# Kernel optimization log

Measured on AMD Instinct MI355X. Metric: run time of the kernel, lower is better.

## Reference

```python
import jax, jax.numpy as jnp
import numpy as np


def setup_inputs() -> dict:
    key = jax.random.key(0)
    k1, k2, k3 = jax.random.split(key, 3)
    n_nodes, d = 1_000_000, 128
    B, L, w, neg_size = 1024, 80, 5, 4
    A = L - w + 1  # 76 anchors per walk
    walk = jax.random.randint(k1, (B, L), 0, n_nodes)
    # torch.randint(low=1, high=n_nodes-1) -> values in [1, n_nodes-2]
    neg = jax.random.randint(k2, (B, A, neg_size), 1, n_nodes - 1)
    embed = jax.random.normal(k3, (n_nodes, d), dtype=jnp.float32)
    return {"walk": walk, "neg": neg, "embed": embed}


def reference(walk, neg, embed):
    B, L = walk.shape
    A = neg.shape[1]          # L - window_size + 1
    w = L - A + 1             # window_size
    anc = walk[:, :A]                                       # [B, A]
    # pos[b, t, i] = walk[b, t + 1 + i], i in [0, w-2]
    sl = jnp.arange(A)[:, None] + jnp.arange(1, w)[None, :]  # [A, w-1]
    pos = walk[:, sl]                                        # [B, A, w-1]
    e_anc = embed[anc]                                       # [B, A, D]
    # fused gather + per-window dot products
    pos_logit = jnp.einsum('bacd,bad->bac', embed[pos], e_anc)  # [B, A, w-1]
    neg_logit = jnp.einsum('bacd,bad->bac', embed[neg], e_anc)  # [B, A, neg]
    # BCEWithLogitsLoss with labels 1 (pos) and 0 (neg), mean over all elements:
    #   label=1 -> softplus(-x);  label=0 -> softplus(x)
    total = pos_logit.size + neg_logit.size
    loss = (jnp.sum(jax.nn.softplus(-pos_logit)) +
            jnp.sum(jax.nn.softplus(neg_logit))) / total
    return loss
```

## Files before the change

### kernel.cpp

```cpp
#include <hip/hip_runtime.h>
#include <math.h>

#define BD   1024
#define LW   80
#define AA   76
#define NEGS 4
#define D    128
#define PAIRS (BD * AA)
#define PAIRS_PER_WAVE 8
#define WAVES_PER_BLOCK 4
#define NBLOCKS (PAIRS / (PAIRS_PER_WAVE * WAVES_PER_BLOCK))

__device__ __forceinline__ float softplus(float x) {
    return fmaxf(x, 0.0f) + log1pf(__expf(-fabsf(x)));
}

__global__ __launch_bounds__(256) void sg_partial(
    const int* __restrict__ walk, const int* __restrict__ neg,
    const float* __restrict__ embed, float* __restrict__ ws)
{
    __shared__ float s_wsum[WAVES_PER_BLOCK];
    const int tid  = threadIdx.x;
    const int wave = tid >> 6;
    const int lane = tid & 63;
    const int gwave = blockIdx.x * WAVES_PER_BLOCK + wave;
    const int pbase = gwave * PAIRS_PER_WAVE;

    float wsum = 0.0f;

    #pragma unroll 1
    for (int i = 0; i < PAIRS_PER_WAVE; ++i) {
        const int p = pbase + i;
        const int b = p / AA;
        const int a = p - b * AA;

        const int* wrow = walk + b * LW + a;
        const int anc = wrow[0];
        const int t0 = wrow[1];
        const int t1 = wrow[2];
        const int t2 = wrow[3];
        const int t3 = wrow[4];
        const int4 nv = *(const int4*)(neg + (size_t)(b * AA + a) * NEGS);

        const size_t loff = (size_t)(lane * 2);
        const float2 ea = *(const float2*)(embed + (size_t)anc * D + loff);

        const float2 e0 = *(const float2*)(embed + (size_t)t0   * D + loff);
        const float2 e1 = *(const float2*)(embed + (size_t)t1   * D + loff);
        const float2 e2 = *(const float2*)(embed + (size_t)t2   * D + loff);
        const float2 e3 = *(const float2*)(embed + (size_t)t3   * D + loff);
        const float2 e4 = *(const float2*)(embed + (size_t)nv.x * D + loff);
        const float2 e5 = *(const float2*)(embed + (size_t)nv.y * D + loff);
        const float2 e6 = *(const float2*)(embed + (size_t)nv.z * D + loff);
        const float2 e7 = *(const float2*)(embed + (size_t)nv.w * D + loff);

        float a0 = fmaf(ea.x, e0.x, ea.y * e0.y);
        float a1 = fmaf(ea.x, e1.x, ea.y * e1.y);
        float a2 = fmaf(ea.x, e2.x, ea.y * e2.y);
        float a3 = fmaf(ea.x, e3.x, ea.y * e3.y);
        float a4 = fmaf(ea.x, e4.x, ea.y * e4.y);
        float a5 = fmaf(ea.x, e5.x, ea.y * e5.y);
        float a6 = fmaf(ea.x, e6.x, ea.y * e6.y);
        float a7 = fmaf(ea.x, e7.x, ea.y * e7.y);

        #pragma unroll
        for (int m = 1; m < 64; m <<= 1) {
            a0 += __shfl_xor(a0, m, 64);
            a1 += __shfl_xor(a1, m, 64);
            a2 += __shfl_xor(a2, m, 64);
            a3 += __shfl_xor(a3, m, 64);
            a4 += __shfl_xor(a4, m, 64);
            a5 += __shfl_xor(a5, m, 64);
            a6 += __shfl_xor(a6, m, 64);
            a7 += __shfl_xor(a7, m, 64);
        }

        wsum += softplus(-a0) + softplus(-a1) + softplus(-a2) + softplus(-a3)
              + softplus( a4) + softplus( a5) + softplus( a6) + softplus( a7);
    }

    if (lane == 0) s_wsum[wave] = wsum;
    __syncthreads();
    if (tid == 0)
        ws[blockIdx.x] = s_wsum[0] + s_wsum[1] + s_wsum[2] + s_wsum[3];
}

__global__ __launch_bounds__(256) void sg_reduce(
    const float* __restrict__ ws, float* __restrict__ out)
{
    __shared__ float s[WAVES_PER_BLOCK];
    const int tid = threadIdx.x;
    float sum = 0.0f;
    for (int i = tid; i < NBLOCKS; i += 256) sum += ws[i];
    #pragma unroll
    for (int m = 1; m < 64; m <<= 1) sum += __shfl_xor(sum, m, 64);
    const int wave = tid >> 6;
    const int lane = tid & 63;
    if (lane == 0) s[wave] = sum;
    __syncthreads();
    if (tid == 0) {
        const float total = (float)((size_t)PAIRS * 8);
        out[0] = (s[0] + s[1] + s[2] + s[3]) * (1.0f / total);
    }
}

extern "C" void kernel_launch(void* const* d_in, const int* in_sizes, int n_in,
                              void* d_out, int out_size, void* d_ws, size_t ws_size,
                              hipStream_t stream) {
    const int*   walk  = (const int*)d_in[0];
    const int*   neg   = (const int*)d_in[1];
    const float* embed = (const float*)d_in[2];
    float* ws  = (float*)d_ws;
    float* out = (float*)d_out;

    sg_partial<<<NBLOCKS, 256, 0, stream>>>(walk, neg, embed, ws);
    sg_reduce<<<1, 256, 0, stream>>>(ws, out);
}
```

Baseline: 651.8 us.

## Map one walk per block and reuse sliding-window embeddings across anchors

Each block now processes a single walk, with each wave handling 19 consecutive anchors and keeping the five window embeddings in a register ring so only one new positive row is gathered per step. The per-pair dot-product reduction is restructured as a transposing butterfly so lanes end up owning one logit each, cutting shuffle count and softplus work per lane. This removes redundant global gathers of overlapping window rows and reduces cross-lane traffic, at the cost of a fully unrolled loop with higher register pressure and less parallel granularity per block.

Measured after the change: 587.7 us. 1.11x faster.

```diff
diff --git a/kernel.cpp b/kernel.cpp
--- a/kernel.cpp
+++ b/kernel.cpp
@@ -7,79 +7,83 @@
 #define NEGS 4
 #define D    128
 #define PAIRS (BD * AA)
-#define PAIRS_PER_WAVE 8
 #define WAVES_PER_BLOCK 4
-#define NBLOCKS (PAIRS / (PAIRS_PER_WAVE * WAVES_PER_BLOCK))
+#define PAIRS_PER_WAVE 19
+#define NBLOCKS BD
 
 __device__ __forceinline__ float softplus(float x) {
     return fmaxf(x, 0.0f) + log1pf(__expf(-fabsf(x)));
 }
 
-__global__ __launch_bounds__(256) void sg_partial(
+__global__ __launch_bounds__(256, 4) void sg_partial(
     const int* __restrict__ walk, const int* __restrict__ neg,
     const float* __restrict__ embed, float* __restrict__ ws)
 {
     __shared__ float s_wsum[WAVES_PER_BLOCK];
     const int tid  = threadIdx.x;
-    const int wave = tid >> 6;
     const int lane = tid & 63;
-    const int gwave = blockIdx.x * WAVES_PER_BLOCK + wave;
-    const int pbase = gwave * PAIRS_PER_WAVE;
+    const int wave = __builtin_amdgcn_readfirstlane(tid >> 6);
+    const int b    = blockIdx.x;
+    const int a0   = wave * PAIRS_PER_WAVE;
+
+    const float* erow = embed + (size_t)(lane * 2);
+    const int*   wrow = walk + b * LW + a0;
+    const int*   nrow = neg + (size_t)(b * AA + a0) * NEGS;
+
+    float2 r[5];
+    #pragma unroll
+    for (int j = 0; j < 5; ++j)
+        r[j] = *(const float2*)(erow + (size_t)wrow[j] * D);
+
+    const bool hi1 = lane & 1;
+    const bool hi2 = lane & 2;
+    const bool hi3 = lane & 4;
 
     float wsum = 0.0f;
 
-    #pragma unroll 1
+    #pragma unroll
     for (int i = 0; i < PAIRS_PER_WAVE; ++i) {
-        const int p = pbase + i;
-        const int b = p / AA;
-        const int a = p - b * AA;
+        const int4 nv = *(const int4*)(nrow + i * NEGS);
+        const float2 e4 = *(const float2*)(erow + (size_t)nv.x * D);
+        const float2 e5 = *(const float2*)(erow + (size_t)nv.y * D);
+        const float2 e6 = *(const float2*)(erow + (size_t)nv.z * D);
+        const float2 e7 = *(const float2*)(erow + (size_t)nv.w * D);
 
-        const int* wrow = walk + b * LW + a;
-        const int anc = wrow[0];
-        const int t0 = wrow[1];
-        const int t1 = wrow[2];
-        const int t2 = wrow[3];
-        const int t3 = wrow[4];
-        const int4 nv = *(const int4*)(neg + (size_t)(b * AA + a) * NEGS);
+        const float2 ea = r[0];
+        float a0v = fmaf(ea.x, r[1].x, ea.y * r[1].y);
+        float a1v = fmaf(ea.x, r[2].x, ea.y * r[2].y);
+        float a2v = fmaf(ea.x, r[3].x, ea.y * r[3].y);
+        float a3v = fmaf(ea.x, r[4].x, ea.y * r[4].y);
+        float a4v = fmaf(ea.x, e4.x,  ea.y * e4.y);
+        float a5v = fmaf(ea.x, e5.x,  ea.y * e5.y);
+        float a6v = fmaf(ea.x, e6.x,  ea.y * e6.y);
+        float a7v = fmaf(ea.x, e7.x,  ea.y * e7.y);
 
-        const size_t loff = (size_t)(lane * 2);
-        const float2 ea = *(const float2*)(embed + (size_t)anc * D + loff);
+        float b0 = (hi1 ? a4v : a0v) + __shfl_xor(hi1 ? a0v : a4v, 1);
+        float b1 = (hi1 ? a5v : a1v) + __shfl_xor(hi1 ? a1v : a5v, 1);
+        float b2 = (hi1 ? a6v : a2v) + __shfl_xor(hi1 ? a2v : a6v, 1);
+        float b3 = (hi1 ? a7v : a3v) + __shfl_xor(hi1 ? a3v : a7v, 1);
 
-        const float2 e0 = *(const float2*)(embed + (size_t)t0   * D + loff);
-        const float2 e1 = *(const float2*)(embed + (size_t)t1   * D + loff);
-        const float2 e2 = *(const float2*)(embed + (size_t)t2   * D + loff);
-        const float2 e3 = *(const float2*)(embed + (size_t)t3   * D + loff);
-        const float2 e4 = *(const float2*)(embed + (size_t)nv.x * D + loff);
-        const float2 e5 = *(const float2*)(embed + (size_t)nv.y * D + loff);
-        const float2 e6 = *(const float2*)(embed + (size_t)nv.z * D + loff);
-        const float2 e7 = *(const float2*)(embed + (size_t)nv.w * D + loff);
+        float c0 = (hi2 ? b2 : b0) + __shfl_xor(hi2 ? b0 : b2, 2);
+        float c1 = (hi2 ? b3 : b1) + __shfl_xor(hi2 ? b1 : b3, 2);
 
-        float a0 = fmaf(ea.x, e0.x, ea.y * e0.y);
-        float a1 = fmaf(ea.x, e1.x, ea.y * e1.y);
-        float a2 = fmaf(ea.x, e2.x, ea.y * e2.y);
-        float a3 = fmaf(ea.x, e3.x, ea.y * e3.y);
-        float a4 = fmaf(ea.x, e4.x, ea.y * e4.y);
-        float a5 = fmaf(ea.x, e5.x, ea.y * e5.y);
-        float a6 = fmaf(ea.x, e6.x, ea.y * e6.y);
-        float a7 = fmaf(ea.x, e7.x, ea.y * e7.y);
+        float dv = (hi3 ? c1 : c0) + __shfl_xor(hi3 ? c0 : c1, 4);
+        dv += __shfl_xor(dv, 8);
+        dv += __shfl_xor(dv, 16);
+        dv += __shfl_xor(dv, 32);
+        wsum += softplus(hi1 ? dv : -dv);
 
-        #pragma unroll
-        for (int m = 1; m < 64; m <<= 1) {
-            a0 += __shfl_xor(a0, m, 64);
-            a1 += __shfl_xor(a1, m, 64);
-            a2 += __shfl_xor(a2, m, 64);
-            a3 += __shfl_xor(a3, m, 64);
-            a4 += __shfl_xor(a4, m, 64);
-            a5 += __shfl_xor(a5, m, 64);
-            a6 += __shfl_xor(a6, m, 64);
-            a7 += __shfl_xor(a7, m, 64);
+        if (i < PAIRS_PER_WAVE - 1) {
+            #pragma unroll
+            for (int j = 0; j < 4; ++j) r[j] = r[j + 1];
+            r[4] = *(const float2*)(erow + (size_t)wrow[i + 5] * D);
         }
-
-        wsum += softplus(-a0) + softplus(-a1) + softplus(-a2) + softplus(-a3)
-              + softplus( a4) + softplus( a5) + softplus( a6) + softplus( a7);
     }
 
-    if (lane == 0) s_wsum[wave] = wsum;
+    #pragma unroll
+    for (int m = 1; m < 64; m <<= 1) wsum += __shfl_xor(wsum, m);
+
+    if (lane == 0) s_wsum[wave] = wsum * 0.125f;
     __syncthreads();
     if (tid == 0)
         ws[blockIdx.x] = s_wsum[0] + s_wsum[1] + s_wsum[2] + s_wsum[3];
@@ -88,12 +92,13 @@
 __global__ __launch_bounds__(256) void sg_reduce(
     const float* __restrict__ ws, float* __restrict__ out)
 {
-    __shared__ float s[WAVES_PER_BLOCK];
+    __shared__ float s[4];
     const int tid = threadIdx.x;
     float sum = 0.0f;
-    for (int i = tid; i < NBLOCKS; i += 256) sum += ws[i];
     #pragma unroll
-    for (int m = 1; m < 64; m <<= 1) sum += __shfl_xor(sum, m, 64);
+    for (int i = 0; i < NBLOCKS / 256; ++i) sum += ws[tid + i * 256];
+    #pragma unroll
+    for (int m = 1; m < 64; m <<= 1) sum += __shfl_xor(sum, m);
     const int wave = tid >> 6;
     const int lane = tid & 63;
     if (lane == 0) s[wave] = sum;
```
